# Kernel tuning notes

Measured on AMD Instinct MI355X. Metric: run time of the kernel, lower is better.

## Reference

```python
import jax, jax.numpy as jnp
import numpy as np

N_NODES = 100000   # vertices
N_EDGES = 20000    # hyperedges
NNZ = 1600000      # incidence entries (avg vertex degree 16)
D_IN = 128
D_OUT = 128


def setup_inputs() -> dict:
    key = jax.random.key(0)
    k1, k2, k3, k4, k5 = jax.random.split(key, 5)
    X = jax.random.normal(k1, (N_NODES, D_IN), dtype=jnp.float32)
    v_idx = jax.random.randint(k2, (NNZ,), 0, N_NODES)
    e_idx = jax.random.randint(k3, (NNZ,), 0, N_EDGES)
    theta_w = jax.random.normal(k4, (D_IN, D_OUT), dtype=jnp.float32) / np.sqrt(D_IN)
    theta_b = jax.random.normal(k5, (D_OUT,), dtype=jnp.float32) * 0.01
    return {"X": X, "theta_w": theta_w, "theta_b": theta_b,
            "v_idx": v_idx, "e_idx": e_idx}


def reference(X, theta_w, theta_b, v_idx, e_idx):
    # degrees (edge weights w_e = 1)
    ones = jnp.ones(v_idx.shape[0], dtype=X.dtype)
    d_v = jax.ops.segment_sum(ones, v_idx, num_segments=N_NODES)   # [N]
    d_e = jax.ops.segment_sum(ones, e_idx, num_segments=N_EDGES)   # [M]
    inv_sqrt_dv = jnp.where(d_v > 0, d_v ** -0.5, 0.0)
    inv_de = jnp.where(d_e > 0, 1.0 / d_e, 0.0)

    # theta: dense GEMM
    Xt = X @ theta_w + theta_b                                     # [N, D_OUT]

    # smoothing_with_HGNN: D_v^{-1/2} H W D_e^{-1} H^T D_v^{-1/2} Xt
    Xs = Xt * inv_sqrt_dv[:, None]                                 # [N, D_OUT]
    Ye = jax.ops.segment_sum(Xs[v_idx], e_idx, num_segments=N_EDGES)  # H^T Xs -> [M, D_OUT]
    Ye = Ye * inv_de[:, None]
    Xv = jax.ops.segment_sum(Ye[e_idx], v_idx, num_segments=N_NODES)  # H Ye -> [N, D_OUT]
    return jax.nn.relu(Xv * inv_sqrt_dv[:, None])
```

## Files before the change

kernel.cpp:

```cpp
#include <hip/hip_runtime.h>

#define N_NODES 100000
#define N_EDGES 20000
#define NNZ     1600000
#define D       128
#define DW      64

#define NB      256
#define CAP_E   8192
#define CAP_V   8192
#define SPAN_E  ((N_EDGES + NB - 1) / NB)
#define SPAN_V  ((N_NODES + NB - 1) / NB)
#define P1_CHUNK 8192
#define P1_BLOCKS ((NNZ + P1_CHUNK - 1) / P1_CHUNK)

__device__ __forceinline__ unsigned int pack_bf2(float lo, float hi) {
  unsigned int ul = __float_as_uint(lo), uh = __float_as_uint(hi);
  ul = (ul + 0x7FFFu + ((ul >> 16) & 1u)) >> 16;
  uh = (uh + 0x7FFFu + ((uh >> 16) & 1u)) & 0xFFFF0000u;
  return ul | uh;
}

__global__ void k_init(int* __restrict__ ce, int* __restrict__ cv) {
  int t = threadIdx.x;
  ce[t] = t * CAP_E;
  cv[t] = t * CAP_V;
}

__global__ __launch_bounds__(256) void k_bin(const int* __restrict__ v_idx, const int* __restrict__ e_idx,
                                             int* __restrict__ ce, int* __restrict__ cv,
                                             unsigned int* __restrict__ Te, unsigned int* __restrict__ Tv) {
  __shared__ int he[NB], hv[NB], be[NB], bv[NB], le[NB], lv[NB];
  int t = threadIdx.x;
  he[t] = 0; hv[t] = 0; le[t] = 0; lv[t] = 0;
  __syncthreads();
  int base = blockIdx.x * P1_CHUNK;
  int v[32], e[32];
#pragma unroll
  for (int j = 0; j < 32; ++j) {
    int idx = base + j * 256 + t;
    if (idx < NNZ) {
      v[j] = v_idx[idx]; e[j] = e_idx[idx];
      atomicAdd(&he[e[j] / SPAN_E], 1);
      atomicAdd(&hv[v[j] / SPAN_V], 1);
    } else v[j] = -1;
  }
  __syncthreads();
  be[t] = he[t] ? atomicAdd(&ce[t], he[t]) : 0;
  bv[t] = hv[t] ? atomicAdd(&cv[t], hv[t]) : 0;
  __syncthreads();
#pragma unroll
  for (int j = 0; j < 32; ++j) {
    if (v[j] < 0) continue;
    int eb = e[j] / SPAN_E, vb = v[j] / SPAN_V;
    int se = be[eb] + atomicAdd(&le[eb], 1);
    int sv = bv[vb] + atomicAdd(&lv[vb], 1);
    if (se < (eb + 1) * CAP_E) Te[se] = ((unsigned)e[j] << 17) | (unsigned)v[j];
    if (sv < (vb + 1) * CAP_V) Tv[sv] = ((unsigned)v[j] << 15) | (unsigned)e[j];
  }
}

__global__ __launch_bounds__(256) void k_sort_v(const int* __restrict__ cv, unsigned int* __restrict__ Tv,
                                                int* __restrict__ cnt_v, float* __restrict__ risv,
                                                int* __restrict__ starts_v) {
  __shared__ unsigned int raw[CAP_V];
  __shared__ int hist[SPAN_V], lcur[SPAN_V], loff[SPAN_V + 1];
  int b = blockIdx.x, t = threadIdx.x;
  int v0 = b * SPAN_V;
  int span = N_NODES - v0; if (span > SPAN_V) span = SPAN_V;
  if (span <= 0) return;
  int n = cv[b] - b * CAP_V; if (n > CAP_V) n = CAP_V; if (n < 0) n = 0;
  for (int i = t; i < n; i += 256) raw[i] = Tv[b * CAP_V + i];
  for (int i = t; i < span; i += 256) { hist[i] = 0; lcur[i] = 0; }
  __syncthreads();
  for (int i = t; i < n; i += 256) atomicAdd(&hist[(int)(raw[i] >> 15) - v0], 1);
  __syncthreads();
  if (t == 0) { int run = 0; for (int i = 0; i < span; ++i) { loff[i] = run; run += hist[i]; } loff[span] = run; }
  __syncthreads();
  for (int i = t; i < n; i += 256) {
    unsigned int p = raw[i];
    int l = (int)(p >> 15) - v0;
    int slot = loff[l] + atomicAdd(&lcur[l], 1);
    Tv[b * CAP_V + slot] = p & 0x7FFFu;
  }
  for (int i = t; i < span; i += 256) {
    int d = hist[i];
    cnt_v[v0 + i] = d;
    risv[v0 + i] = d > 0 ? rsqrtf((float)d) : 0.0f;
    starts_v[v0 + i] = b * CAP_V + loff[i];
  }
}

__global__ __launch_bounds__(256) void k_sort_e(const int* __restrict__ ce, unsigned int* __restrict__ Te,
                                                const float* __restrict__ risv,
                                                int* __restrict__ cnt_e, float* __restrict__ invde,
                                                int* __restrict__ starts_e, float* __restrict__ qv) {
  __shared__ unsigned int raw[CAP_E];
  __shared__ int hist[SPAN_E], lcur[SPAN_E], loff[SPAN_E + 1];
  __shared__ float qacc[SPAN_E];
  int b = blockIdx.x, t = threadIdx.x;
  int e0 = b * SPAN_E;
  int span = N_EDGES - e0; if (span > SPAN_E) span = SPAN_E;
  if (span <= 0) return;
  int n = ce[b] - b * CAP_E; if (n > CAP_E) n = CAP_E; if (n < 0) n = 0;
  for (int i = t; i < n; i += 256) raw[i] = Te[b * CAP_E + i];
  for (int i = t; i < span; i += 256) { hist[i] = 0; lcur[i] = 0; qacc[i] = 0.f; }
  __syncthreads();
  for (int i = t; i < n; i += 256) atomicAdd(&hist[(int)(raw[i] >> 17) - e0], 1);
  __syncthreads();
  if (t == 0) { int run = 0; for (int i = 0; i < span; ++i) { loff[i] = run; run += hist[i]; } loff[span] = run; }
  __syncthreads();
  for (int i = t; i < n; i += 256) {
    unsigned int p = raw[i];
    int l = (int)(p >> 17) - e0;
    int vtx = (int)(p & 0x1FFFFu);
    int slot = loff[l] + atomicAdd(&lcur[l], 1);
    Te[b * CAP_E + slot] = (unsigned)vtx;
    atomicAdd(&qacc[l], risv[vtx]);
  }
  __syncthreads();
  for (int i = t; i < span; i += 256) {
    int d = hist[i];
    cnt_e[e0 + i] = d;
    invde[e0 + i] = d > 0 ? 1.0f / (float)d : 0.0f;
    starts_e[e0 + i] = b * CAP_E + loff[i];
    qv[e0 + i] = qacc[i];
  }
}

__global__ __launch_bounds__(256) void k_prescale(const float* __restrict__ X, const float* __restrict__ risv,
                                                  unsigned int* __restrict__ Xs) {
  int p = blockIdx.x * 256 + threadIdx.x;
  if (p >= N_NODES * DW) return;
  int v = p >> 6;
  float r = risv[v];
  float2 x = *(const float2*)(X + (size_t)p * 2);
  Xs[p] = pack_bf2(r * x.x, r * x.y);
}

__global__ void k_edge_gather(const unsigned int* __restrict__ Xs,
                              const int* __restrict__ starts_e, const int* __restrict__ cnt_e,
                              const unsigned int* __restrict__ members,
                              unsigned int* __restrict__ Qeb) {
  int wid = (blockIdx.x * 256 + threadIdx.x) >> 6;
  int lane = threadIdx.x & 63;
  if (wid >= N_EDGES) return;
  int beg = __builtin_amdgcn_readfirstlane(starts_e[wid]);
  int end = beg + __builtin_amdgcn_readfirstlane(cnt_e[wid]);
  float ax = 0.f, ay = 0.f;
  int i = beg;
  for (; i + 16 <= end; i += 16) {
    int vv[16]; unsigned int xx[16];
#pragma unroll
    for (int j = 0; j < 16; ++j) vv[j] = members[i + j];
#pragma unroll
    for (int j = 0; j < 16; ++j) xx[j] = Xs[(size_t)vv[j] * DW + lane];
#pragma unroll
    for (int j = 0; j < 16; ++j) {
      ax += __uint_as_float(xx[j] << 16);
      ay += __uint_as_float(xx[j] & 0xFFFF0000u);
    }
  }
  if (i + 8 <= end) {
    int vv[8]; unsigned int xx[8];
#pragma unroll
    for (int j = 0; j < 8; ++j) vv[j] = members[i + j];
#pragma unroll
    for (int j = 0; j < 8; ++j) xx[j] = Xs[(size_t)vv[j] * DW + lane];
#pragma unroll
    for (int j = 0; j < 8; ++j) {
      ax += __uint_as_float(xx[j] << 16);
      ay += __uint_as_float(xx[j] & 0xFFFF0000u);
    }
    i += 8;
  }
  for (; i < end; ++i) {
    unsigned int x = Xs[(size_t)members[i] * DW + lane];
    ax += __uint_as_float(x << 16);
    ay += __uint_as_float(x & 0xFFFF0000u);
  }
  Qeb[(size_t)wid * DW + lane] = pack_bf2(ax, ay);
}

__global__ __launch_bounds__(256) void k_gemm(const unsigned int* __restrict__ Qeb, const float* __restrict__ qv,
                                              const float* __restrict__ W, const float* __restrict__ bias,
                                              const float* __restrict__ invde, unsigned int* __restrict__ Yeb) {
  __shared__ float Wl[D * D];
  __shared__ float bl[D];
  __shared__ float Ql[16][130];
  int tid = threadIdx.x;
  const float4* W4 = (const float4*)W;
  float4* Wl4 = (float4*)Wl;
#pragma unroll
  for (int j = 0; j < 16; ++j) Wl4[tid + 256 * j] = W4[tid + 256 * j];
  if (tid < 32) ((float4*)bl)[tid] = ((const float4*)bias)[tid];
  int row0 = blockIdx.x * 16;
  const unsigned int* Q8 = Qeb + (size_t)row0 * DW;
#pragma unroll
  for (int j = 0; j < 4; ++j) {
    int idx = tid + 256 * j;
    int r = idx >> 6, c = idx & 63;
    unsigned int u = Q8[idx];
    Ql[r][2 * c]     = __uint_as_float(u << 16);
    Ql[r][2 * c + 1] = __uint_as_float(u & 0xFFFF0000u);
  }
  __syncthreads();
  int ty = tid >> 4, tx = tid & 15;
  float acc[8];
#pragma unroll
  for (int j = 0; j < 8; ++j) acc[j] = 0.f;
#pragma unroll 4
  for (int k = 0; k < D; ++k) {
    float xv = Ql[ty][k];
    const float* wr = Wl + k * D + tx * 8;
#pragma unroll
    for (int j = 0; j < 8; ++j) acc[j] += xv * wr[j];
  }
  int row = row0 + ty;
  float s = invde[row]; float q = qv[row];
  unsigned int* orow = Yeb + (size_t)row * DW + tx * 4;
#pragma unroll
  for (int j = 0; j < 4; ++j) {
    float lo = s * (acc[2 * j]     + q * bl[tx * 8 + 2 * j]);
    float hi = s * (acc[2 * j + 1] + q * bl[tx * 8 + 2 * j + 1]);
    orow[j] = pack_bf2(lo, hi);
  }
}

__global__ void k_vertex_gather(const unsigned int* __restrict__ Yeb, const float* __restrict__ risv,
                                const int* __restrict__ starts_v, const int* __restrict__ cnt_v,
                                const unsigned int* __restrict__ members,
                                float* __restrict__ out) {
  int wid = (blockIdx.x * 256 + threadIdx.x) >> 6;
  int lane = threadIdx.x & 63;
  if (wid >= N_NODES) return;
  int beg = __builtin_amdgcn_readfirstlane(starts_v[wid]);
  int end = beg + __builtin_amdgcn_readfirstlane(cnt_v[wid]);
  float ax = 0.f, ay = 0.f;
  int i = beg;
  for (; i + 8 <= end; i += 8) {
    int ee[8]; unsigned int yy[8];
#pragma unroll
    for (int j = 0; j < 8; ++j) ee[j] = members[i + j];
#pragma unroll
    for (int j = 0; j < 8; ++j) yy[j] = Yeb[(size_t)ee[j] * DW + lane];
#pragma unroll
    for (int j = 0; j < 8; ++j) {
      ax += __uint_as_float(yy[j] << 16);
      ay += __uint_as_float(yy[j] & 0xFFFF0000u);
    }
  }
  for (; i < end; ++i) {
    unsigned int y = Yeb[(size_t)members[i] * DW + lane];
    ax += __uint_as_float(y << 16);
    ay += __uint_as_float(y & 0xFFFF0000u);
  }
  float s = risv[wid];
  float2 o; o.x = fmaxf(ax * s, 0.f); o.y = fmaxf(ay * s, 0.f);
  *(float2*)(out + (size_t)wid * D + lane * 2) = o;
}

extern "C" void kernel_launch(void* const* d_in, const int* in_sizes, int n_in,
                              void* d_out, int out_size, void* d_ws, size_t ws_size,
                              hipStream_t stream) {
  const float* X    = (const float*)d_in[0];
  const float* W    = (const float*)d_in[1];
  const float* bias = (const float*)d_in[2];
  const int* v_idx  = (const int*)d_in[3];
  const int* e_idx  = (const int*)d_in[4];
  float* out = (float*)d_out;

  char* p = (char*)d_ws;
  auto alloc = [&](size_t bytes) { char* r = p; p += (bytes + 255) & ~(size_t)255; return r; };
  unsigned int* Te  = (unsigned int*)alloc((size_t)NB * CAP_E * 4);
  unsigned int* Tv  = (unsigned int*)alloc((size_t)NB * CAP_V * 4);
  unsigned int* Xs  = (unsigned int*)alloc((size_t)N_NODES * DW * 4);
  unsigned int* Qeb = (unsigned int*)alloc((size_t)N_EDGES * DW * 4);
  unsigned int* Yeb = (unsigned int*)alloc((size_t)N_EDGES * DW * 4);
  float* qv    = (float*)alloc((size_t)N_EDGES * 4);
  float* risv  = (float*)alloc((size_t)N_NODES * 4);
  float* invde = (float*)alloc((size_t)N_EDGES * 4);
  int* cnt_e    = (int*)alloc((size_t)N_EDGES * 4);
  int* cnt_v    = (int*)alloc((size_t)N_NODES * 4);
  int* starts_e = (int*)alloc((size_t)N_EDGES * 4);
  int* starts_v = (int*)alloc((size_t)N_NODES * 4);
  int* ce       = (int*)alloc(NB * 4);
  int* cv       = (int*)alloc(NB * 4);

  k_init<<<1, NB, 0, stream>>>(ce, cv);
  k_bin<<<P1_BLOCKS, 256, 0, stream>>>(v_idx, e_idx, ce, cv, Te, Tv);
  k_sort_v<<<NB, 256, 0, stream>>>(cv, Tv, cnt_v, risv, starts_v);
  k_sort_e<<<NB, 256, 0, stream>>>(ce, Te, risv, cnt_e, invde, starts_e, qv);
  k_prescale<<<(N_NODES * DW + 255) / 256, 256, 0, stream>>>(X, risv, Xs);

  k_edge_gather<<<N_EDGES / 4, 256, 0, stream>>>(Xs, starts_e, cnt_e, Te, Qeb);
  k_gemm<<<N_EDGES / 16, 256, 0, stream>>>(Qeb, qv, W, bias, invde, Yeb);
  k_vertex_gather<<<N_NODES / 4, 256, 0, stream>>>(Yeb, risv, starts_v, cnt_v, Tv, out);
}
```

Before: 307.6 us.

## Fuse vertex prescale into vertex sort, shrink bin chunk, unroll vertex gather

```diff
diff --git a/kernel.cpp b/kernel.cpp
--- a/kernel.cpp
+++ b/kernel.cpp
@@ -11,7 +11,8 @@
 #define CAP_V   8192
 #define SPAN_E  ((N_EDGES + NB - 1) / NB)
 #define SPAN_V  ((N_NODES + NB - 1) / NB)
-#define P1_CHUNK 8192
+#define P1_CHUNK 2048
+#define P1_ITER  (P1_CHUNK / 256)
 #define P1_BLOCKS ((NNZ + P1_CHUNK - 1) / P1_CHUNK)
 
 __device__ __forceinline__ unsigned int pack_bf2(float lo, float hi) {
@@ -35,9 +36,9 @@
   he[t] = 0; hv[t] = 0; le[t] = 0; lv[t] = 0;
   __syncthreads();
   int base = blockIdx.x * P1_CHUNK;
-  int v[32], e[32];
-#pragma unroll
-  for (int j = 0; j < 32; ++j) {
+  int v[P1_ITER], e[P1_ITER];
+#pragma unroll
+  for (int j = 0; j < P1_ITER; ++j) {
     int idx = base + j * 256 + t;
     if (idx < NNZ) {
       v[j] = v_idx[idx]; e[j] = e_idx[idx];
@@ -50,7 +51,7 @@
   bv[t] = hv[t] ? atomicAdd(&cv[t], hv[t]) : 0;
   __syncthreads();
 #pragma unroll
-  for (int j = 0; j < 32; ++j) {
+  for (int j = 0; j < P1_ITER; ++j) {
     if (v[j] < 0) continue;
     int eb = e[j] / SPAN_E, vb = v[j] / SPAN_V;
     int se = be[eb] + atomicAdd(&le[eb], 1);
@@ -62,9 +63,11 @@
 
 __global__ __launch_bounds__(256) void k_sort_v(const int* __restrict__ cv, unsigned int* __restrict__ Tv,
                                                 int* __restrict__ cnt_v, float* __restrict__ risv,
-                                                int* __restrict__ starts_v) {
+                                                int* __restrict__ starts_v,
+                                                const float* __restrict__ X, unsigned int* __restrict__ Xs) {
   __shared__ unsigned int raw[CAP_V];
   __shared__ int hist[SPAN_V], lcur[SPAN_V], loff[SPAN_V + 1];
+  __shared__ float rv[SPAN_V];
   int b = blockIdx.x, t = threadIdx.x;
   int v0 = b * SPAN_V;
   int span = N_NODES - v0; if (span > SPAN_V) span = SPAN_V;
@@ -85,9 +88,20 @@
   }
   for (int i = t; i < span; i += 256) {
     int d = hist[i];
+    float r = d > 0 ? rsqrtf((float)d) : 0.0f;
     cnt_v[v0 + i] = d;
-    risv[v0 + i] = d > 0 ? rsqrtf((float)d) : 0.0f;
+    risv[v0 + i] = r;
+    rv[i] = r;
     starts_v[v0 + i] = b * CAP_V + loff[i];
+  }
+  __syncthreads();
+  int total = span * DW;
+  for (int idx = t; idx < total; idx += 256) {
+    int vl = idx >> 6;
+    float r = rv[vl];
+    size_t gp = (size_t)(v0 + vl) * DW + (idx & 63);
+    float2 x = *(const float2*)(X + gp * 2);
+    Xs[gp] = pack_bf2(r * x.x, r * x.y);
   }
 }
 
@@ -128,16 +142,6 @@
   }
 }
 
-__global__ __launch_bounds__(256) void k_prescale(const float* __restrict__ X, const float* __restrict__ risv,
-                                                  unsigned int* __restrict__ Xs) {
-  int p = blockIdx.x * 256 + threadIdx.x;
-  if (p >= N_NODES * DW) return;
-  int v = p >> 6;
-  float r = risv[v];
-  float2 x = *(const float2*)(X + (size_t)p * 2);
-  Xs[p] = pack_bf2(r * x.x, r * x.y);
-}
-
 __global__ void k_edge_gather(const unsigned int* __restrict__ Xs,
                               const int* __restrict__ starts_e, const int* __restrict__ cnt_e,
                               const unsigned int* __restrict__ members,
@@ -238,7 +242,19 @@
   int end = beg + __builtin_amdgcn_readfirstlane(cnt_v[wid]);
   float ax = 0.f, ay = 0.f;
   int i = beg;
-  for (; i + 8 <= end; i += 8) {
+  for (; i + 16 <= end; i += 16) {
+    int ee[16]; unsigned int yy[16];
+#pragma unroll
+    for (int j = 0; j < 16; ++j) ee[j] = members[i + j];
+#pragma unroll
+    for (int j = 0; j < 16; ++j) yy[j] = Yeb[(size_t)ee[j] * DW + lane];
+#pragma unroll
+    for (int j = 0; j < 16; ++j) {
+      ax += __uint_as_float(yy[j] << 16);
+      ay += __uint_as_float(yy[j] & 0xFFFF0000u);
+    }
+  }
+  if (i + 8 <= end) {
     int ee[8]; unsigned int yy[8];
 #pragma unroll
     for (int j = 0; j < 8; ++j) ee[j] = members[i + j];
@@ -249,6 +265,7 @@
       ax += __uint_as_float(yy[j] << 16);
       ay += __uint_as_float(yy[j] & 0xFFFF0000u);
     }
+    i += 8;
   }
   for (; i < end; ++i) {
     unsigned int y = Yeb[(size_t)members[i] * DW + lane];
@@ -289,9 +306,8 @@
 
   k_init<<<1, NB, 0, stream>>>(ce, cv);
   k_bin<<<P1_BLOCKS, 256, 0, stream>>>(v_idx, e_idx, ce, cv, Te, Tv);
-  k_sort_v<<<NB, 256, 0, stream>>>(cv, Tv, cnt_v, risv, starts_v);
+  k_sort_v<<<NB, 256, 0, stream>>>(cv, Tv, cnt_v, risv, starts_v, X, Xs);
   k_sort_e<<<NB, 256, 0, stream>>>(ce, Te, risv, cnt_e, invde, starts_e, qv);
-  k_prescale<<<(N_NODES * DW + 255) / 256, 256, 0, stream>>>(X, risv, Xs);
 
   k_edge_gather<<<N_EDGES / 4, 256, 0, stream>>>(Xs, starts_e, cnt_e, Te, Qeb);
   k_gemm<<<N_EDGES / 16, 256, 0, stream>>>(Qeb, qv, W, bias, invde, Yeb);
```

Result: slower. 317.8 us (+3.3%).
